# Optimization experiments

Hardware: AMD Instinct MI355X
Metric: run time of the kernel (lower is better)

## Reference

```python
import jax, jax.numpy as jnp
import numpy as np

K = 2            # top-k experts
TEMP = 1.0       # temperature
LN_EPS = 1e-5

def setup_inputs() -> dict:
    key = jax.random.key(0)
    B, S, D, E = 4, 4096, 2048, 64
    k0, k1, k2, k3 = jax.random.split(key, 4)
    x = jax.random.normal(k0, (B, S, D), dtype=jnp.float32)
    Wg = jax.random.normal(k1, (E, D), dtype=jnp.float32) * 0.02       # base_gate weight [out,in]
    gamma = jnp.ones((D,), jnp.float32)                                 # LayerNorm weight
    beta = jnp.zeros((D,), jnp.float32)                                 # LayerNorm bias
    W1 = jax.random.normal(k2, (D // 2, D), dtype=jnp.float32) * 0.02   # diff_pred linear1
    W2 = jax.random.normal(k3, (1, D // 2), dtype=jnp.float32) * 0.02   # diff_pred linear2
    return {"x": x, "Wg": Wg, "gamma": gamma, "beta": beta, "W1": W1, "W2": W2}

def reference(x, Wg, gamma, beta, W1, W2):
    # base expert logits: [B,S,E]
    logits = jnp.einsum('bsd,ed->bse', x, Wg)
    # difficulty predictor: LN -> Linear -> GELU -> Linear -> sigmoid, [B,S,1]
    mu = jnp.mean(x, axis=-1, keepdims=True)
    var = jnp.var(x, axis=-1, keepdims=True)
    h = (x - mu) * jax.lax.rsqrt(var + LN_EPS) * gamma + beta
    h1 = jax.nn.gelu(jnp.einsum('bsd,hd->bsh', h, W1), approximate=False)
    diff = jax.nn.sigmoid(jnp.einsum('bsh,oh->bso', h1, W2))
    # modulate + temperature (eval mode: no jitter / mask_drop)
    logits = logits / (1.0 + diff) * (1.0 / TEMP)
    probs_soft = jax.nn.softmax(logits, axis=-1)
    # top-k selection
    _, idx = jax.lax.top_k(logits, K)                    # [B,S,K]
    hard_any = jnp.max(jax.nn.one_hot(idx, logits.shape[-1], dtype=probs_soft.dtype), axis=2)  # [B,S,E]
    probs_st = hard_any - probs_soft + probs_soft        # faithful to source (no detach)
    scores = jnp.take_along_axis(probs_st, idx, axis=-1)  # [B,S,K]
    scores = scores / jnp.maximum(jnp.sum(scores, axis=-1, keepdims=True), 1e-9)
    importance = jax.lax.stop_gradient(jnp.mean(probs_soft, axis=(0, 1)))  # [E]
    load = jax.lax.stop_gradient(jnp.mean(hard_any, axis=(0, 1)))          # [E]
    return (idx, scores, probs_soft, importance, load)
```

## Files before the change

### kernel.cpp

```cpp
#include <hip/hip_runtime.h>
#include <math.h>

#define BS_TOK 16384
#define DIM    2048
#define NEXP   64
#define DHID   1024
#define GKS    4
#define KSL    (DIM / GKS)

typedef __attribute__((ext_vector_type(8))) _Float16 f16x8;
typedef __attribute__((ext_vector_type(4))) float    f32x4;

#define GLOBAL_AS const __attribute__((address_space(1))) void*
#define LDS_AS    __attribute__((address_space(3))) void*

__device__ __forceinline__ float gelu_f(float x) {
  return 0.5f * x * (1.0f + erff(x * 0.70710678118654752440f));
}

__global__ __launch_bounds__(256) void ln_kernel(const float* __restrict__ X,
                                                 const float* __restrict__ gamma,
                                                 const float* __restrict__ beta,
                                                 _Float16* __restrict__ H) {
  const int tid  = threadIdx.x;
  const int w    = tid >> 6, lane = tid & 63;
  const int t    = blockIdx.x * 4 + w;
  const float* xr = X + (size_t)t * DIM;
  float4 xv[8];
#pragma unroll
  for (int j = 0; j < 4; ++j) {
    const int c0 = (j * 64 + lane) * 8;
    xv[j * 2]     = *(const float4*)(xr + c0);
    xv[j * 2 + 1] = *(const float4*)(xr + c0 + 4);
  }
  float s = 0.f, q = 0.f;
#pragma unroll
  for (int j = 0; j < 8; ++j) {
    s += (xv[j].x + xv[j].y) + (xv[j].z + xv[j].w);
    q += (xv[j].x * xv[j].x + xv[j].y * xv[j].y) + (xv[j].z * xv[j].z + xv[j].w * xv[j].w);
  }
#pragma unroll
  for (int off = 32; off > 0; off >>= 1) {
    s += __shfl_xor(s, off);
    q += __shfl_xor(q, off);
  }
  const float mu  = s * (1.0f / DIM);
  const float var = q * (1.0f / DIM) - mu * mu;
  const float rs  = rsqrtf(var + 1e-5f);
#pragma unroll
  for (int j = 0; j < 4; ++j) {
    const int c0 = (j * 64 + lane) * 8;
    const float4 g0 = *(const float4*)(gamma + c0);
    const float4 g1 = *(const float4*)(gamma + c0 + 4);
    const float4 b0 = *(const float4*)(beta + c0);
    const float4 b1 = *(const float4*)(beta + c0 + 4);
    const float4 a = xv[j * 2], b = xv[j * 2 + 1];
    f16x8 h;
    h[0] = (_Float16)((a.x - mu) * rs * g0.x + b0.x);
    h[1] = (_Float16)((a.y - mu) * rs * g0.y + b0.y);
    h[2] = (_Float16)((a.z - mu) * rs * g0.z + b0.z);
    h[3] = (_Float16)((a.w - mu) * rs * g0.w + b0.w);
    h[4] = (_Float16)((b.x - mu) * rs * g1.x + b1.x);
    h[5] = (_Float16)((b.y - mu) * rs * g1.y + b1.y);
    h[6] = (_Float16)((b.z - mu) * rs * g1.z + b1.z);
    h[7] = (_Float16)((b.w - mu) * rs * g1.w + b1.w);
    *(f16x8*)(H + (size_t)t * DIM + c0) = h;
  }
}

__global__ __launch_bounds__(256) void w1cast_kernel(const float* __restrict__ W1,
                                                     _Float16* __restrict__ W1h) {
  const int i = (blockIdx.x * 256 + threadIdx.x) * 8;
  const float4 a = *(const float4*)(W1 + i);
  const float4 b = *(const float4*)(W1 + i + 4);
  f16x8 o;
  o[0] = (_Float16)a.x; o[1] = (_Float16)a.y; o[2] = (_Float16)a.z; o[3] = (_Float16)a.w;
  o[4] = (_Float16)b.x; o[5] = (_Float16)b.y; o[6] = (_Float16)b.z; o[7] = (_Float16)b.w;
  *(f16x8*)(W1h + i) = o;
}

__global__ __launch_bounds__(256) void gate_kernel(const float* __restrict__ X,
                                                   const float* __restrict__ Wg,
                                                   float* __restrict__ logitsP) {
  __shared__ float sX[16][68];
  __shared__ float sW[16][68];
  const int tid  = threadIdx.x;
  const int m0   = blockIdx.x * 64;
  const int k0   = blockIdx.y * KSL;
  const int srow = tid >> 2;
  const int skq  = tid & 3;
  const int ty   = tid >> 4;
  const int tx   = tid & 15;
  const float* xb = X  + (size_t)(m0 + srow) * DIM + k0 + skq * 4;
  const float* wb = Wg + (size_t)srow * DIM + k0 + skq * 4;
  float acc[4][4] = {};
  float4 rx = *(const float4*)xb;
  float4 rw = *(const float4*)wb;
  for (int kt = 0; kt < KSL; kt += 16) {
    __syncthreads();
    sX[skq * 4 + 0][srow] = rx.x;
    sX[skq * 4 + 1][srow] = rx.y;
    sX[skq * 4 + 2][srow] = rx.z;
    sX[skq * 4 + 3][srow] = rx.w;
    sW[skq * 4 + 0][srow] = rw.x;
    sW[skq * 4 + 1][srow] = rw.y;
    sW[skq * 4 + 2][srow] = rw.z;
    sW[skq * 4 + 3][srow] = rw.w;
    const int ktn = (kt + 16 < KSL) ? kt + 16 : 0;
    rx = *(const float4*)(xb + ktn);
    rw = *(const float4*)(wb + ktn);
    __syncthreads();
#pragma unroll
    for (int k = 0; k < 16; ++k) {
      const float4 a4 = *(const float4*)&sX[k][ty * 4];
      const float4 b4 = *(const float4*)&sW[k][tx * 4];
      const float av[4] = {a4.x, a4.y, a4.z, a4.w};
      const float bv[4] = {b4.x, b4.y, b4.z, b4.w};
#pragma unroll
      for (int i = 0; i < 4; ++i)
#pragma unroll
        for (int j = 0; j < 4; ++j) acc[i][j] += av[i] * bv[j];
    }
  }
  float* op = logitsP + (size_t)blockIdx.y * (BS_TOK * NEXP)
            + (size_t)(m0 + ty * 4) * NEXP + tx * 4;
#pragma unroll
  for (int i = 0; i < 4; ++i) {
    float4 o;
    o.x = acc[i][0]; o.y = acc[i][1]; o.z = acc[i][2]; o.w = acc[i][3];
    *(float4*)(op + (size_t)i * NEXP) = o;
  }
}

__global__ __launch_bounds__(256) void g2_kernel(const _Float16* __restrict__ H,
                                                 const _Float16* __restrict__ W1h,
                                                 const float* __restrict__ W2,
                                                 float* __restrict__ diffz) {
  __shared__ __align__(16) _Float16 sA[128 * 32];
  __shared__ __align__(16) _Float16 sB[128 * 32];
  const int bid = blockIdx.x;
  const int c   = bid & 7;
  const int j   = bid >> 3;
  const int m0  = (c * 16 + (j >> 3)) * 128;
  const int n0  = (j & 7) * 128;
  const int tid  = threadIdx.x;
  const int w    = tid >> 6, lane = tid & 63;
  const int wr   = w >> 1,  wc   = w & 1;
  const int col  = lane & 15, quad = lane >> 4;
  const int row0 = tid >> 2,  kp = tid & 3;
  const int row1 = row0 + 64;
  const _Float16* gA0 = H   + (size_t)(m0 + row0) * DIM + kp * 8;
  const _Float16* gA1 = H   + (size_t)(m0 + row1) * DIM + kp * 8;
  const _Float16* gB0 = W1h + (size_t)(n0 + row0) * DIM + kp * 8;
  const _Float16* gB1 = W1h + (size_t)(n0 + row1) * DIM + kp * 8;
  f32x4 acc[4][4] = {};
  for (int kt = 0; kt < DIM; kt += 32) {
    __syncthreads();
    __builtin_amdgcn_global_load_lds((GLOBAL_AS)(gA0 + kt), (LDS_AS)(sA + tid * 8), 16, 0, 0);
    __builtin_amdgcn_global_load_lds((GLOBAL_AS)(gA1 + kt), (LDS_AS)(sA + (256 + tid) * 8), 16, 0, 0);
    __builtin_amdgcn_global_load_lds((GLOBAL_AS)(gB0 + kt), (LDS_AS)(sB + tid * 8), 16, 0, 0);
    __builtin_amdgcn_global_load_lds((GLOBAL_AS)(gB1 + kt), (LDS_AS)(sB + (256 + tid) * 8), 16, 0, 0);
    __syncthreads();
    f16x8 af[4], bf[4];
#pragma unroll
    for (int mi = 0; mi < 4; ++mi)
      af[mi] = *(const f16x8*)(sA + (wr * 64 + mi * 16 + col) * 32 + quad * 8);
#pragma unroll
    for (int ni = 0; ni < 4; ++ni)
      bf[ni] = *(const f16x8*)(sB + (wc * 64 + ni * 16 + col) * 32 + quad * 8);
#pragma unroll
    for (int mi = 0; mi < 4; ++mi)
#pragma unroll
      for (int ni = 0; ni < 4; ++ni)
        acc[mi][ni] = __builtin_amdgcn_mfma_f32_16x16x32_f16(af[mi], bf[ni], acc[mi][ni], 0, 0, 0);
  }
  float w2v[4];
#pragma unroll
  for (int ni = 0; ni < 4; ++ni) w2v[ni] = W2[n0 + wc * 64 + ni * 16 + col];
#pragma unroll
  for (int mi = 0; mi < 4; ++mi) {
#pragma unroll
    for (int reg = 0; reg < 4; ++reg) {
      float v = 0.f;
#pragma unroll
      for (int ni = 0; ni < 4; ++ni) v += gelu_f(acc[mi][ni][reg]) * w2v[ni];
      v += __shfl_xor(v, 1);
      v += __shfl_xor(v, 2);
      v += __shfl_xor(v, 4);
      v += __shfl_xor(v, 8);
      if (col == 0)
        atomicAdd(diffz + m0 + wr * 64 + mi * 16 + quad * 4 + reg, v);
    }
  }
}

__global__ __launch_bounds__(256) void finalize_kernel(const float* __restrict__ logitsP,
                                                       const float* __restrict__ diffz,
                                                       float* __restrict__ out_idx,
                                                       float* __restrict__ out_scores,
                                                       float* __restrict__ out_probs,
                                                       float* __restrict__ imp_acc,
                                                       float* __restrict__ load_acc) {
  const int tid  = threadIdx.x;
  const int w    = tid >> 6, lane = tid & 63;
  const size_t PS = (size_t)BS_TOK * NEXP;
  float acc_imp = 0.f, acc_load = 0.f;
  for (int it = 0; it < 8; ++it) {
    const int t    = blockIdx.x * 32 + it * 4 + w;
    const float* lp = logitsP + (size_t)t * NEXP + lane;
    const float L  = ((lp[0] + lp[PS]) + lp[2 * PS]) + lp[3 * PS];
    const float z  = diffz[t];
    const float d  = 1.0f / (1.0f + expf(-z));
    const float l  = L / (1.0f + d);
    float m = l;
#pragma unroll
    for (int off = 32; off > 0; off >>= 1) m = fmaxf(m, __shfl_xor(m, off));
    float p = expf(l - m);
    float s = p;
#pragma unroll
    for (int off = 32; off > 0; off >>= 1) s += __shfl_xor(s, off);
    p /= s;
    float v = l; int bi = lane;
#pragma unroll
    for (int off = 32; off > 0; off >>= 1) {
      const float ov = __shfl_xor(v, off);
      const int   oi = __shfl_xor(bi, off);
      if (ov > v || (ov == v && oi < bi)) { v = ov; bi = oi; }
    }
    const int i1 = bi;
    float v2 = (lane == i1) ? -INFINITY : l;
    int bi2 = lane;
#pragma unroll
    for (int off = 32; off > 0; off >>= 1) {
      const float ov = __shfl_xor(v2, off);
      const int   oi = __shfl_xor(bi2, off);
      if (ov > v2 || (ov == v2 && oi < bi2)) { v2 = ov; bi2 = oi; }
    }
    const int i2 = bi2;
    const float p1 = __shfl(p, i1);
    const float p2 = __shfl(p, i2);
    const float s1 = (1.0f - p1) + p1;
    const float s2 = (1.0f - p2) + p2;
    const float den = fmaxf(s1 + s2, 1e-9f);
    if (lane == 0) {
      out_idx[t * 2]        = (float)i1;
      out_idx[t * 2 + 1]    = (float)i2;
      out_scores[t * 2]     = s1 / den;
      out_scores[t * 2 + 1] = s2 / den;
    }
    out_probs[(size_t)t * NEXP + lane] = p;
    acc_imp  += p;
    acc_load += (lane == i1 || lane == i2) ? 1.0f : 0.0f;
  }
  __shared__ float s_imp[256];
  __shared__ float s_hard[256];
  s_imp[tid]  = acc_imp;
  s_hard[tid] = acc_load;
  __syncthreads();
  if (tid < 64) {
    const float si = s_imp[tid] + s_imp[64 + tid] + s_imp[128 + tid] + s_imp[192 + tid];
    const float sl = s_hard[tid] + s_hard[64 + tid] + s_hard[128 + tid] + s_hard[192 + tid];
    atomicAdd(imp_acc + tid, si);
    atomicAdd(load_acc + tid, sl);
  }
}

__global__ void scale_kernel(const float* __restrict__ acc,
                             float* __restrict__ out_imp,
                             float* __restrict__ out_load) {
  const int tid = threadIdx.x;
  const float inv = 1.0f / 16384.0f;
  if (tid < 64)       out_imp[tid]        = acc[tid] * inv;
  else if (tid < 128) out_load[tid - 64]  = acc[tid] * inv;
}

extern "C" void kernel_launch(void* const* d_in, const int* in_sizes, int n_in,
                              void* d_out, int out_size, void* d_ws, size_t ws_size,
                              hipStream_t stream) {
  (void)in_sizes; (void)n_in; (void)out_size; (void)ws_size;
  const float* X     = (const float*)d_in[0];
  const float* Wg    = (const float*)d_in[1];
  const float* gamma = (const float*)d_in[2];
  const float* beta  = (const float*)d_in[3];
  const float* W1    = (const float*)d_in[4];
  const float* W2    = (const float*)d_in[5];
  float* out = (float*)d_out;

  char* ws = (char*)d_ws;
  _Float16* H       = (_Float16*)(ws);
  _Float16* W1h     = (_Float16*)(ws + 67108864ull);
  float*    logitsP = (float*)  (ws + 71303168ull);
  float*    diffz   = (float*)  (ws + 88080384ull);
  float*    accs    = (float*)  (ws + 88145920ull);

  float* out_idx    = out;
  float* out_scores = out + 32768;
  float* out_probs  = out + 65536;
  float* out_imp    = out + 1114112;
  float* out_load   = out + 1114176;

  hipMemsetAsync(diffz, 0, 65536ull + 512ull, stream);
  ln_kernel<<<BS_TOK / 4, 256, 0, stream>>>(X, gamma, beta, H);
  w1cast_kernel<<<(DHID * DIM) / (256 * 8), 256, 0, stream>>>(W1, W1h);
  gate_kernel<<<dim3(BS_TOK / 64, GKS), 256, 0, stream>>>(X, Wg, logitsP);
  g2_kernel<<<(DHID / 128) * (BS_TOK / 128), 256, 0, stream>>>(H, W1h, W2, diffz);
  finalize_kernel<<<BS_TOK / 32, 256, 0, stream>>>(logitsP, diffz, out_idx, out_scores,
                                                   out_probs, accs, accs + 64);
  scale_kernel<<<1, 128, 0, stream>>>(accs, out_imp, out_load);
}
```

Before: 414.2 us.

## Double-buffer g2 LDS loads and enlarge gate kernel register tile

```diff
diff --git a/kernel.cpp b/kernel.cpp
--- a/kernel.cpp
+++ b/kernel.cpp
@@ -79,56 +79,74 @@
   *(f16x8*)(W1h + i) = o;
 }
 
-__global__ __launch_bounds__(256) void gate_kernel(const float* __restrict__ X,
+#define GT_M 128
+#define PX   132
+#define PW   68
+__global__ __launch_bounds__(128) void gate_kernel(const float* __restrict__ X,
                                                    const float* __restrict__ Wg,
                                                    float* __restrict__ logitsP) {
-  __shared__ float sX[16][68];
-  __shared__ float sW[16][68];
+  __shared__ float sX[16][PX];
+  __shared__ float sW[16][PW];
   const int tid  = threadIdx.x;
-  const int m0   = blockIdx.x * 64;
+  const int m0   = blockIdx.x * GT_M;
   const int k0   = blockIdx.y * KSL;
   const int srow = tid >> 2;
   const int skq  = tid & 3;
-  const int ty   = tid >> 4;
-  const int tx   = tid & 15;
+  const int ty   = tid >> 3;
+  const int tx   = tid & 7;
   const float* xb = X  + (size_t)(m0 + srow) * DIM + k0 + skq * 4;
   const float* wb = Wg + (size_t)srow * DIM + k0 + skq * 4;
-  float acc[4][4] = {};
-  float4 rx = *(const float4*)xb;
-  float4 rw = *(const float4*)wb;
+  float acc[8][8] = {};
+  float4 rx[4], rw[2];
+#pragma unroll
+  for (int r = 0; r < 4; ++r) rx[r] = *(const float4*)(xb + (size_t)(r * 32) * DIM);
+#pragma unroll
+  for (int r = 0; r < 2; ++r) rw[r] = *(const float4*)(wb + (size_t)(r * 32) * DIM);
   for (int kt = 0; kt < KSL; kt += 16) {
     __syncthreads();
-    sX[skq * 4 + 0][srow] = rx.x;
-    sX[skq * 4 + 1][srow] = rx.y;
-    sX[skq * 4 + 2][srow] = rx.z;
-    sX[skq * 4 + 3][srow] = rx.w;
-    sW[skq * 4 + 0][srow] = rw.x;
-    sW[skq * 4 + 1][srow] = rw.y;
-    sW[skq * 4 + 2][srow] = rw.z;
-    sW[skq * 4 + 3][srow] = rw.w;
+#pragma unroll
+    for (int r = 0; r < 4; ++r) {
+      sX[skq * 4 + 0][srow + r * 32] = rx[r].x;
+      sX[skq * 4 + 1][srow + r * 32] = rx[r].y;
+      sX[skq * 4 + 2][srow + r * 32] = rx[r].z;
+      sX[skq * 4 + 3][srow + r * 32] = rx[r].w;
+    }
+#pragma unroll
+    for (int r = 0; r < 2; ++r) {
+      sW[skq * 4 + 0][srow + r * 32] = rw[r].x;
+      sW[skq * 4 + 1][srow + r * 32] = rw[r].y;
+      sW[skq * 4 + 2][srow + r * 32] = rw[r].z;
+      sW[skq * 4 + 3][srow + r * 32] = rw[r].w;
+    }
     const int ktn = (kt + 16 < KSL) ? kt + 16 : 0;
-    rx = *(const float4*)(xb + ktn);
-    rw = *(const float4*)(wb + ktn);
+#pragma unroll
+    for (int r = 0; r < 4; ++r) rx[r] = *(const float4*)(xb + (size_t)(r * 32) * DIM + ktn);
+#pragma unroll
+    for (int r = 0; r < 2; ++r) rw[r] = *(const float4*)(wb + (size_t)(r * 32) * DIM + ktn);
     __syncthreads();
 #pragma unroll
     for (int k = 0; k < 16; ++k) {
-      const float4 a4 = *(const float4*)&sX[k][ty * 4];
-      const float4 b4 = *(const float4*)&sW[k][tx * 4];
-      const float av[4] = {a4.x, a4.y, a4.z, a4.w};
-      const float bv[4] = {b4.x, b4.y, b4.z, b4.w};
-#pragma unroll
-      for (int i = 0; i < 4; ++i)
-#pragma unroll
-        for (int j = 0; j < 4; ++j) acc[i][j] += av[i] * bv[j];
-    }
-  }
-  float* op = logitsP + (size_t)blockIdx.y * (BS_TOK * NEXP)
-            + (size_t)(m0 + ty * 4) * NEXP + tx * 4;
-#pragma unroll
-  for (int i = 0; i < 4; ++i) {
-    float4 o;
-    o.x = acc[i][0]; o.y = acc[i][1]; o.z = acc[i][2]; o.w = acc[i][3];
-    *(float4*)(op + (size_t)i * NEXP) = o;
+      const float4 a0 = *(const float4*)&sX[k][ty * 8];
+      const float4 a1 = *(const float4*)&sX[k][ty * 8 + 4];
+      const float4 b0 = *(const float4*)&sW[k][tx * 8];
+      const float4 b1 = *(const float4*)&sW[k][tx * 8 + 4];
+      const float av[8] = {a0.x, a0.y, a0.z, a0.w, a1.x, a1.y, a1.z, a1.w};
+      const float bv[8] = {b0.x, b0.y, b0.z, b0.w, b1.x, b1.y, b1.z, b1.w};
+#pragma unroll
+      for (int i = 0; i < 8; ++i)
+#pragma unroll
+        for (int j = 0; j < 8; ++j) acc[i][j] += av[i] * bv[j];
+    }
+  }
+  float* op = logitsP + (size_t)blockIdx.y * ((size_t)BS_TOK * NEXP)
+            + (size_t)(m0 + ty * 8) * NEXP + tx * 8;
+#pragma unroll
+  for (int i = 0; i < 8; ++i) {
+    float4 o0, o1;
+    o0.x = acc[i][0]; o0.y = acc[i][1]; o0.z = acc[i][2]; o0.w = acc[i][3];
+    o1.x = acc[i][4]; o1.y = acc[i][5]; o1.z = acc[i][6]; o1.w = acc[i][7];
+    *(float4*)(op + (size_t)i * NEXP)     = o0;
+    *(float4*)(op + (size_t)i * NEXP + 4) = o1;
   }
 }
 
@@ -136,8 +154,8 @@
                                                  const _Float16* __restrict__ W1h,
                                                  const float* __restrict__ W2,
                                                  float* __restrict__ diffz) {
-  __shared__ __align__(16) _Float16 sA[128 * 32];
-  __shared__ __align__(16) _Float16 sB[128 * 32];
+  __shared__ __align__(16) _Float16 sA[2][128 * 32];
+  __shared__ __align__(16) _Float16 sB[2][128 * 32];
   const int bid = blockIdx.x;
   const int c   = bid & 7;
   const int j   = bid >> 3;
@@ -154,25 +172,32 @@
   const _Float16* gB0 = W1h + (size_t)(n0 + row0) * DIM + kp * 8;
   const _Float16* gB1 = W1h + (size_t)(n0 + row1) * DIM + kp * 8;
   f32x4 acc[4][4] = {};
+#define G2_STAGE(buf, off)                                                                              \
+  do {                                                                                                  \
+    __builtin_amdgcn_global_load_lds((GLOBAL_AS)(gA0 + (off)), (LDS_AS)(sA[buf] + tid * 8), 16, 0, 0);  \
+    __builtin_amdgcn_global_load_lds((GLOBAL_AS)(gA1 + (off)), (LDS_AS)(sA[buf] + (256 + tid) * 8), 16, 0, 0); \
+    __builtin_amdgcn_global_load_lds((GLOBAL_AS)(gB0 + (off)), (LDS_AS)(sB[buf] + tid * 8), 16, 0, 0);  \
+    __builtin_amdgcn_global_load_lds((GLOBAL_AS)(gB1 + (off)), (LDS_AS)(sB[buf] + (256 + tid) * 8), 16, 0, 0); \
+  } while (0)
+  G2_STAGE(0, 0);
+  __syncthreads();
+  int cur = 0;
   for (int kt = 0; kt < DIM; kt += 32) {
-    __syncthreads();
-    __builtin_amdgcn_global_load_lds((GLOBAL_AS)(gA0 + kt), (LDS_AS)(sA + tid * 8), 16, 0, 0);
-    __builtin_amdgcn_global_load_lds((GLOBAL_AS)(gA1 + kt), (LDS_AS)(sA + (256 + tid) * 8), 16, 0, 0);
-    __builtin_amdgcn_global_load_lds((GLOBAL_AS)(gB0 + kt), (LDS_AS)(sB + tid * 8), 16, 0, 0);
-    __builtin_amdgcn_global_load_lds((GLOBAL_AS)(gB1 + kt), (LDS_AS)(sB + (256 + tid) * 8), 16, 0, 0);
-    __syncthreads();
+    if (kt + 32 < DIM) G2_STAGE(cur ^ 1, kt + 32);
     f16x8 af[4], bf[4];
 #pragma unroll
     for (int mi = 0; mi < 4; ++mi)
-      af[mi] = *(const f16x8*)(sA + (wr * 64 + mi * 16 + col) * 32 + quad * 8);
+      af[mi] = *(const f16x8*)(sA[cur] + (wr * 64 + mi * 16 + col) * 32 + quad * 8);
 #pragma unroll
     for (int ni = 0; ni < 4; ++ni)
-      bf[ni] = *(const f16x8*)(sB + (wc * 64 + ni * 16 + col) * 32 + quad * 8);
+      bf[ni] = *(const f16x8*)(sB[cur] + (wc * 64 + ni * 16 + col) * 32 + quad * 8);
 #pragma unroll
     for (int mi = 0; mi < 4; ++mi)
 #pragma unroll
       for (int ni = 0; ni < 4; ++ni)
         acc[mi][ni] = __builtin_amdgcn_mfma_f32_16x16x32_f16(af[mi], bf[ni], acc[mi][ni], 0, 0, 0);
+    __syncthreads();
+    cur ^= 1;
   }
   float w2v[4];
 #pragma unroll
@@ -302,7 +327,7 @@
   hipMemsetAsync(diffz, 0, 65536ull + 512ull, stream);
   ln_kernel<<<BS_TOK / 4, 256, 0, stream>>>(X, gamma, beta, H);
   w1cast_kernel<<<(DHID * DIM) / (256 * 8), 256, 0, stream>>>(W1, W1h);
-  gate_kernel<<<dim3(BS_TOK / 64, GKS), 256, 0, stream>>>(X, Wg, logitsP);
+  gate_kernel<<<dim3(BS_TOK / GT_M, GKS), 128, 0, stream>>>(X, Wg, logitsP);
   g2_kernel<<<(DHID / 128) * (BS_TOK / 128), 256, 0, stream>>>(H, W1h, W2, diffz);
   finalize_kernel<<<BS_TOK / 32, 256, 0, stream>>>(logitsP, diffz, out_idx, out_scores,
                                                    out_probs, accs, accs + 64);
```

Measured after the change: 430.9 us. 4.0% more time.

## Enlarge g2 GEMM tiles to 256x256 with triple-buffered async LDS loads and swizzle

Applied to the files above, without the earlier changes.

```diff
diff --git a/kernel.cpp b/kernel.cpp
--- a/kernel.cpp
+++ b/kernel.cpp
@@ -132,53 +132,74 @@
   }
 }
 
-__global__ __launch_bounds__(256) void g2_kernel(const _Float16* __restrict__ H,
-                                                 const _Float16* __restrict__ W1h,
-                                                 const float* __restrict__ W2,
-                                                 float* __restrict__ diffz) {
-  __shared__ __align__(16) _Float16 sA[128 * 32];
-  __shared__ __align__(16) _Float16 sB[128 * 32];
+#define G2BM 256
+#define G2BN 256
+#define G2BK 32
+#define G2NS (DIM / G2BK)
+
+__global__ __launch_bounds__(512, 2) void g2_kernel(const _Float16* __restrict__ H,
+                                                    const _Float16* __restrict__ W1h,
+                                                    const float* __restrict__ W2,
+                                                    float* __restrict__ diffz) {
+  __shared__ __align__(16) _Float16 sA[3][G2BM * G2BK];
+  __shared__ __align__(16) _Float16 sB[3][G2BN * G2BK];
   const int bid = blockIdx.x;
-  const int c   = bid & 7;
-  const int j   = bid >> 3;
-  const int m0  = (c * 16 + (j >> 3)) * 128;
-  const int n0  = (j & 7) * 128;
+  const int m0  = (bid >> 2) * G2BM;
+  const int n0  = (bid & 3) * G2BN;
   const int tid  = threadIdx.x;
-  const int w    = tid >> 6, lane = tid & 63;
-  const int wr   = w >> 1,  wc   = w & 1;
+  const int lane = tid & 63;
+  const int w    = tid >> 6;
+  const int wr   = w >> 2, wc = w & 3;
   const int col  = lane & 15, quad = lane >> 4;
-  const int row0 = tid >> 2,  kp = tid & 3;
-  const int row1 = row0 + 64;
-  const _Float16* gA0 = H   + (size_t)(m0 + row0) * DIM + kp * 8;
-  const _Float16* gA1 = H   + (size_t)(m0 + row1) * DIM + kp * 8;
-  const _Float16* gB0 = W1h + (size_t)(n0 + row0) * DIM + kp * 8;
-  const _Float16* gB1 = W1h + (size_t)(n0 + row1) * DIM + kp * 8;
-  f32x4 acc[4][4] = {};
-  for (int kt = 0; kt < DIM; kt += 32) {
-    __syncthreads();
-    __builtin_amdgcn_global_load_lds((GLOBAL_AS)(gA0 + kt), (LDS_AS)(sA + tid * 8), 16, 0, 0);
-    __builtin_amdgcn_global_load_lds((GLOBAL_AS)(gA1 + kt), (LDS_AS)(sA + (256 + tid) * 8), 16, 0, 0);
-    __builtin_amdgcn_global_load_lds((GLOBAL_AS)(gB0 + kt), (LDS_AS)(sB + tid * 8), 16, 0, 0);
-    __builtin_amdgcn_global_load_lds((GLOBAL_AS)(gB1 + kt), (LDS_AS)(sB + (256 + tid) * 8), 16, 0, 0);
-    __syncthreads();
-    f16x8 af[4], bf[4];
-#pragma unroll
-    for (int mi = 0; mi < 4; ++mi)
-      af[mi] = *(const f16x8*)(sA + (wr * 64 + mi * 16 + col) * 32 + quad * 8);
+  const int srow = tid >> 2;
+  const int ks   = (tid & 3) ^ ((tid >> 3) & 3);
+  const _Float16* gA0 = H   + (size_t)(m0 + srow)       * DIM + ks * 8;
+  const _Float16* gA1 = H   + (size_t)(m0 + 128 + srow) * DIM + ks * 8;
+  const _Float16* gB0 = W1h + (size_t)(n0 + srow)       * DIM + ks * 8;
+  const _Float16* gB1 = W1h + (size_t)(n0 + 128 + srow) * DIM + ks * 8;
+  const int sq = (quad ^ ((col >> 1) & 3)) * 8;
+  f32x4 acc[8][4] = {};
+#define G2_STAGE(bf_, kt_)                                                                                   \
+  do {                                                                                                       \
+    __builtin_amdgcn_global_load_lds((GLOBAL_AS)(gA0 + (kt_)), (LDS_AS)(sA[bf_] + tid * 8), 16, 0, 0);       \
+    __builtin_amdgcn_global_load_lds((GLOBAL_AS)(gA1 + (kt_)), (LDS_AS)(sA[bf_] + 128 * G2BK + tid * 8), 16, 0, 0); \
+    __builtin_amdgcn_global_load_lds((GLOBAL_AS)(gB0 + (kt_)), (LDS_AS)(sB[bf_] + tid * 8), 16, 0, 0);       \
+    __builtin_amdgcn_global_load_lds((GLOBAL_AS)(gB1 + (kt_)), (LDS_AS)(sB[bf_] + 128 * G2BK + tid * 8), 16, 0, 0); \
+  } while (0)
+  G2_STAGE(0, 0);
+  G2_STAGE(1, G2BK);
+  int cur = 0, pf = 2;
+  for (int s = 0; s < G2NS; ++s) {
+    if (s == G2NS - 1) asm volatile("s_waitcnt vmcnt(0)" ::: "memory");
+    else               asm volatile("s_waitcnt vmcnt(4)" ::: "memory");
+    __builtin_amdgcn_s_barrier();
+    if (s + 2 < G2NS) G2_STAGE(pf, (s + 2) * G2BK);
+    const _Float16* A = sA[cur];
+    const _Float16* B = sB[cur];
+    f16x8 af[8], bf[4];
+#pragma unroll
+    for (int mi = 0; mi < 8; ++mi)
+      af[mi] = *(const f16x8*)(A + (wr * 128 + mi * 16 + col) * G2BK + sq);
 #pragma unroll
     for (int ni = 0; ni < 4; ++ni)
-      bf[ni] = *(const f16x8*)(sB + (wc * 64 + ni * 16 + col) * 32 + quad * 8);
-#pragma unroll
-    for (int mi = 0; mi < 4; ++mi)
+      bf[ni] = *(const f16x8*)(B + (wc * 64 + ni * 16 + col) * G2BK + sq);
+    __builtin_amdgcn_s_setprio(1);
+#pragma unroll
+    for (int mi = 0; mi < 8; ++mi)
 #pragma unroll
       for (int ni = 0; ni < 4; ++ni)
         acc[mi][ni] = __builtin_amdgcn_mfma_f32_16x16x32_f16(af[mi], bf[ni], acc[mi][ni], 0, 0, 0);
-  }
+    __builtin_amdgcn_s_setprio(0);
+    asm volatile("s_waitcnt lgkmcnt(0)" ::: "memory");
+    cur = (cur == 2) ? 0 : cur + 1;
+    pf  = (pf  == 2) ? 0 : pf  + 1;
+  }
+#undef G2_STAGE
   float w2v[4];
 #pragma unroll
   for (int ni = 0; ni < 4; ++ni) w2v[ni] = W2[n0 + wc * 64 + ni * 16 + col];
 #pragma unroll
-  for (int mi = 0; mi < 4; ++mi) {
+  for (int mi = 0; mi < 8; ++mi) {
 #pragma unroll
     for (int reg = 0; reg < 4; ++reg) {
       float v = 0.f;
@@ -189,7 +210,7 @@
       v += __shfl_xor(v, 4);
       v += __shfl_xor(v, 8);
       if (col == 0)
-        atomicAdd(diffz + m0 + wr * 64 + mi * 16 + quad * 4 + reg, v);
+        atomicAdd(diffz + m0 + wr * 128 + mi * 16 + quad * 4 + reg, v);
     }
   }
 }
@@ -303,7 +324,7 @@
   ln_kernel<<<BS_TOK / 4, 256, 0, stream>>>(X, gamma, beta, H);
   w1cast_kernel<<<(DHID * DIM) / (256 * 8), 256, 0, stream>>>(W1, W1h);
   gate_kernel<<<dim3(BS_TOK / 64, GKS), 256, 0, stream>>>(X, Wg, logitsP);
-  g2_kernel<<<(DHID / 128) * (BS_TOK / 128), 256, 0, stream>>>(H, W1h, W2, diffz);
+  g2_kernel<<<(DHID / G2BN) * (BS_TOK / G2BM), 512, 0, stream>>>(H, W1h, W2, diffz);
   finalize_kernel<<<BS_TOK / 32, 256, 0, stream>>>(logitsP, diffz, out_idx, out_scores,
                                                    out_probs, accs, accs + 64);
   scale_kernel<<<1, 128, 0, stream>>>(accs, out_imp, out_load);
```

Result: no change. 415.2 us (+0.2%).
